# Kernel tuning notes

Hardware: AMD Instinct MI355X
Metric: run time of the kernel (lower is better)

The kernel has to match this reference:

```python
import jax, jax.numpy as jnp
import numpy as np

B, S, D = 2, 2048, 4096
H, KV, HD = 32, 8, 128
THETA = 10000.0


def rotate_half(x):
    x1, x2 = x[..., : HD // 2], x[..., HD // 2 :]
    return jnp.concatenate((-x2, x1), axis=-1)


def setup_inputs() -> dict:
    key = jax.random.key(0)
    ks = jax.random.split(key, 8)
    s = 1.0 / np.sqrt(D)
    return {
        "hidden_states": jax.random.normal(ks[0], (B, S, D), jnp.float32),
        "modality_indicators": jax.random.randint(ks[1], (B, S), 0, 2, jnp.int64 if jax.config.jax_enable_x64 else jnp.int32),
        "position_ids": jnp.arange(S, dtype=jnp.int32),
        "Wq": jax.random.normal(ks[2], (D, H * HD), jnp.float32) * s,
        "Wk0": jax.random.normal(ks[3], (D, KV * HD), jnp.float32) * s,
        "Wk1": jax.random.normal(ks[4], (D, KV * HD), jnp.float32) * s,
        "Wv0": jax.random.normal(ks[5], (D, KV * HD), jnp.float32) * s,
        "Wv1": jax.random.normal(ks[6], (D, KV * HD), jnp.float32) * s,
        "Wo": jax.random.normal(ks[7], (H * HD, D), jnp.float32) * s,
    }


def reference(hidden_states, modality_indicators, position_ids, Wq, Wk0, Wk1, Wv0, Wv1, Wo):
    x = hidden_states
    # Multiway (modality-routed) k/v projections: per-token select between two linears.
    sel = (modality_indicators == 1)[..., None]  # [B,S,1]
    q = x @ Wq                                   # [B,S,H*HD]
    k = jnp.where(sel, x @ Wk1, x @ Wk0)         # [B,S,KV*HD]
    v = jnp.where(sel, x @ Wv1, x @ Wv0)

    q = q.reshape(B, S, H, HD).transpose(0, 2, 1, 3)    # [B,H,S,HD]
    k = k.reshape(B, S, KV, HD).transpose(0, 2, 1, 3)   # [B,KV,S,HD]
    v = v.reshape(B, S, KV, HD).transpose(0, 2, 1, 3)

    # RoPE cache and application (emb = cat(freqs, freqs))
    inv_freq = 1.0 / (THETA ** (jnp.arange(0, HD, 2, dtype=jnp.float32) / HD))
    freqs = position_ids.astype(jnp.float32)[:, None] * inv_freq[None, :]   # [S,HD/2]
    emb = jnp.concatenate((freqs, freqs), axis=-1)                          # [S,HD]
    cos = jnp.cos(emb)[None, None, :, :]                                    # [1,1,S,HD]
    sin = jnp.sin(emb)[None, None, :, :]
    q = q * cos + rotate_half(q) * sin
    k = k * cos + rotate_half(k) * sin

    # GQA: repeat kv heads
    n_rep = H // KV
    k = jnp.repeat(k, n_rep, axis=1)  # [B,H,S,HD]
    v = jnp.repeat(v, n_rep, axis=1)

    scores = jnp.einsum("bhqd,bhkd->bhqk", q, k) / np.sqrt(HD)
    causal = jnp.tril(jnp.ones((S, S), dtype=bool))
    scores = jnp.where(causal[None, None], scores, jnp.finfo(scores.dtype).min)
    attn = jax.nn.softmax(scores, axis=-1)
    ctx = jnp.einsum("bhqk,bhkd->bhqd", attn, v)            # [B,H,S,HD]
    ctx = ctx.transpose(0, 2, 1, 3).reshape(B, S, H * HD)
    return ctx @ Wo
```

## Files before the change

kernel.cpp:

```cpp
#include <hip/hip_runtime.h>

typedef unsigned short u16;
typedef unsigned int   u32;
using bf16x8 = __attribute__((ext_vector_type(8))) __bf16;
using f32x4  = __attribute__((ext_vector_type(4))) float;
using f32x16 = __attribute__((ext_vector_type(16))) float;
using u32x4  = __attribute__((ext_vector_type(4))) unsigned int;


__device__ __forceinline__ u16 f2bf(float f) {
  u32 u = __builtin_bit_cast(u32, f);
  return (u16)((u + 0x7fffu + ((u >> 16) & 1u)) >> 16);
}
__device__ __forceinline__ float bf2f(u16 h) {
  return __builtin_bit_cast(float, (u32)h << 16);
}
__device__ __forceinline__ f32x4 mfma16(bf16x8 a, bf16x8 b, f32x4 c) {
  return __builtin_amdgcn_mfma_f32_16x16x32_bf16(a, b, c, 0, 0, 0);
}
__device__ __forceinline__ f32x16 mfma32(bf16x8 a, bf16x8 b, f32x16 c) {
  return __builtin_amdgcn_mfma_f32_32x32x16_bf16(a, b, c, 0, 0, 0);
}
__device__ __forceinline__ f32x16 zero16() {
  f32x16 z;
#pragma unroll
  for (int i = 0; i < 16; ++i) z[i] = 0.f;
  return z;
}
__device__ __forceinline__ void g2l16(const void* gp, void* lp) {
  __builtin_amdgcn_global_load_lds(
      (__attribute__((address_space(1))) void*)(void*)gp,
      (__attribute__((address_space(3))) void*)lp, 16, 0, 0);
}

__global__ void k_cvt(const float* __restrict__ in, u16* __restrict__ out, int n4) {
  int i = blockIdx.x * 256 + threadIdx.x;
  if (i >= n4) return;
  float4 v = ((const float4*)in)[i];
  ushort4 o;
  o.x = f2bf(v.x); o.y = f2bf(v.y); o.z = f2bf(v.z); o.w = f2bf(v.w);
  ((ushort4*)out)[i] = o;
}

__global__ void k_tcvt(const float* __restrict__ in, u16* __restrict__ out, int K, int N) {
  __shared__ u16 t[32][33];
  int n0 = blockIdx.x * 32, k0 = blockIdx.y * 32;
  int r = threadIdx.x >> 3, c4 = (threadIdx.x & 7) * 4;
  float4 v = *(const float4*)(in + (size_t)(k0 + r) * N + n0 + c4);
  t[c4 + 0][r] = f2bf(v.x);
  t[c4 + 1][r] = f2bf(v.y);
  t[c4 + 2][r] = f2bf(v.z);
  t[c4 + 3][r] = f2bf(v.w);
  __syncthreads();
  ushort4 o;
  o.x = t[r][c4 + 0]; o.y = t[r][c4 + 1]; o.z = t[r][c4 + 2]; o.w = t[r][c4 + 3];
  *(ushort4*)(out + (size_t)(n0 + r) * K + k0 + c4) = o;
}

__global__ void k_scan(const int* __restrict__ mod, int* __restrict__ perm, int* __restrict__ meta) {
  __shared__ int ps[1024];
  const int b = blockIdx.x, t = threadIdx.x;
  perm[b * 2304 + t] = -1;
  perm[b * 2304 + 1024 + t] = -1;
  if (t < 256) perm[b * 2304 + 2048 + t] = -1;
  const int i0 = 2 * t, i1 = 2 * t + 1;
  const int f0 = (mod[b * 2048 + i0] != 1) ? 1 : 0;
  const int f1 = (mod[b * 2048 + i1] != 1) ? 1 : 0;
  const int sum = f0 + f1;
  ps[t] = sum;
  __syncthreads();
  for (int off = 1; off < 1024; off <<= 1) {
    int v = (t >= off) ? ps[t - off] : 0;
    __syncthreads();
    ps[t] += v;
    __syncthreads();
  }
  const int total0 = ps[1023];
  const int excl = ps[t] - sum;
  const int nt0 = (total0 + 255) >> 8;
  const int off1 = nt0 * 256;
  const int s0 = f0 ? excl : off1 + (i0 - excl);
  const int s1 = f1 ? (excl + f0) : off1 + (i1 - (excl + f0));
  perm[b * 2304 + s0] = i0;
  perm[b * 2304 + s1] = i1;
  if (t == 0) { meta[b * 2] = total0; meta[b * 2 + 1] = nt0; }
}

#define TILE_BODY(T, VMLIT, DOSTAGE)                                         \
  {                                                                          \
    asm volatile("s_waitcnt vmcnt(" VMLIT ")" ::: "memory");                 \
    __builtin_amdgcn_s_barrier();                                            \
    __builtin_amdgcn_sched_barrier(0);                                       \
    const u16* base_ = lds + ((T) & 3) * 16384;                              \
    bf16x8 bfr[4], afr[4];                                                   \
    _Pragma("unroll")                                                        \
    for (int nf = 0; nf < 4; ++nf)                                           \
      bfr[nf] = *(const bf16x8*)(base_ + boff + nf * 512);                   \
    _Pragma("unroll")                                                        \
    for (int mf = 0; mf < 4; ++mf)                                           \
      afr[mf] = *(const bf16x8*)(base_ + aoff + mf * 512);                   \
    if (DOSTAGE) stage((T) + 3);                                             \
    __builtin_amdgcn_s_setprio(1);                                           \
    _Pragma("unroll")                                                        \
    for (int mf = 0; mf < 4; ++mf)                                           \
      _Pragma("unroll")                                                      \
      for (int nf = 0; nf < 4; ++nf)                                         \
        acc[mf][nf] = mfma16(afr[mf], bfr[nf], acc[mf][nf]);                 \
    __builtin_amdgcn_s_setprio(0);                                           \
    _Pragma("unroll")                                                        \
    for (int mf = 0; mf < 4; ++mf)                                           \
      afr[mf] = *(const bf16x8*)(base_ + aoff + (mf + 4) * 512);             \
    __builtin_amdgcn_s_setprio(1);                                           \
    _Pragma("unroll")                                                        \
    for (int mf = 0; mf < 4; ++mf)                                           \
      _Pragma("unroll")                                                      \
      for (int nf = 0; nf < 4; ++nf)                                         \
        acc[mf + 4][nf] = mfma16(afr[mf], bfr[nf], acc[mf + 4][nf]);         \
    __builtin_amdgcn_s_setprio(0);                                           \
  }

template <int MODE>
__global__ __launch_bounds__(512, 2) void k_gemm8(const u16* __restrict__ A, const u16* __restrict__ Bt,
                                                  void* __restrict__ Cp, int NH) {
  __shared__ u16 lds[4 * 16384];
  const int tid = threadIdx.x, wid = tid >> 6, l = tid & 63, g = l >> 4, li = l & 15;
  const int wr = wid >> 2, wc = wid & 3;
  const int bid = blockIdx.x;
  const int swz = (bid & 7) * 32 + (bid >> 3);
  const int m0 = (swz >> 4) * 256, n0 = (swz & 15) * 256;

  const int bo = wid * 2048 + l * 16;
  const int srow = bo >> 6;
  const int sgg = (l & 3) ^ ((l >> 3) & 3);
  const u16* ApA = A + (size_t)(m0 + srow) * 4096 + sgg * 8;
  const u16* ApB = Bt + (size_t)(n0 + srow) * 4096 + sgg * 8;

  auto stage = [&](int t) {
    const u16* a = ApA + t * 32;
    const u16* b = ApB + t * 32;
    u16* da = (u16*)lds + (t & 3) * 16384 + wid * 1024;
    u16* db = da + 8192;
    g2l16(a, da);
    g2l16(a + (size_t)16 * 4096, da + 512);
    g2l16(b, db);
    g2l16(b + (size_t)16 * 4096, db + 512);
  };

  const int lsl8 = (g ^ ((li >> 1) & 3)) * 8;
  const int aoff = (wr * 128 + li) * 32 + lsl8;
  const int boff = 8192 + (wc * 64 + li) * 32 + lsl8;

  const f32x4 vzero = {0.f, 0.f, 0.f, 0.f};
  f32x4 acc[8][4];
#pragma unroll
  for (int m = 0; m < 8; ++m)
#pragma unroll
    for (int n = 0; n < 4; ++n) acc[m][n] = vzero;

  stage(0); stage(1); stage(2);
  for (int t = 0; t < 125; ++t) TILE_BODY(t, "8", true);
  TILE_BODY(125, "8", false);
  TILE_BODY(126, "4", false);
  TILE_BODY(127, "0", false);

  (void)NH;
#pragma unroll
  for (int mf = 0; mf < 8; ++mf)
#pragma unroll
    for (int nf = 0; nf < 4; ++nf)
#pragma unroll
      for (int j = 0; j < 4; ++j) {
        int row = m0 + wr * 128 + mf * 16 + g * 4 + j;
        int col = n0 + wc * 64 + nf * 16 + li;
        float v = acc[mf][nf][j];
        if constexpr (MODE == 2) {
          ((float*)Cp)[(size_t)row * 4096 + col] = v;
        } else if constexpr (MODE == 1) {
          int b = row >> 11, s = row & 2047, h = col >> 7, d = col & 127;
          ((u16*)Cp)[(((size_t)(b * NH + h)) * 2048 + s) * 128 + d] = f2bf(v);
        }
      }
}

__global__ __launch_bounds__(512, 2) void k_gemmkv(const u16* __restrict__ Xb,
                                                   const u16* __restrict__ B0, const u16* __restrict__ B1,
                                                   const int* __restrict__ perm, const int* __restrict__ meta,
                                                   u16* __restrict__ Ksel, u16* __restrict__ Vsel) {
  __shared__ u16 lds[4 * 16384];
  const int tid = threadIdx.x, wid = tid >> 6, l = tid & 63, g = l >> 4, li = l & 15;
  const int wr = wid >> 2, wc = wid & 3;
  const int bb = blockIdx.y / 9, tm = blockIdx.y % 9;
  const int n0 = blockIdx.x * 256;
  const int nt0 = meta[bb * 2 + 1];
  const u16* Bt = (tm >= nt0) ? B1 : B0;

  const int bo = wid * 2048 + l * 16;
  const int srow = bo >> 6;
  const int sgg = (l & 3) ^ ((l >> 3) & 3);
  int t0 = perm[bb * 2304 + tm * 256 + srow];
  int t1 = perm[bb * 2304 + tm * 256 + srow + 16];
  if (t0 < 0) t0 = 0;
  if (t1 < 0) t1 = 0;
  const u16* ApA0 = Xb + ((size_t)bb * 2048 + t0) * 4096 + sgg * 8;
  const u16* ApA1 = Xb + ((size_t)bb * 2048 + t1) * 4096 + sgg * 8;
  const u16* ApB = Bt + (size_t)(n0 + srow) * 4096 + sgg * 8;

  auto stage = [&](int t) {
    u16* da = (u16*)lds + (t & 3) * 16384 + wid * 1024;
    u16* db = da + 8192;
    g2l16(ApA0 + t * 32, da);
    g2l16(ApA1 + t * 32, da + 512);
    g2l16(ApB + t * 32, db);
    g2l16(ApB + (size_t)16 * 4096 + t * 32, db + 512);
  };

  const int lsl8 = (g ^ ((li >> 1) & 3)) * 8;
  const int aoff = (wr * 128 + li) * 32 + lsl8;
  const int boff = 8192 + (wc * 64 + li) * 32 + lsl8;

  const f32x4 vzero = {0.f, 0.f, 0.f, 0.f};
  f32x4 acc[8][4];
#pragma unroll
  for (int m = 0; m < 8; ++m)
#pragma unroll
    for (int n = 0; n < 4; ++n) acc[m][n] = vzero;

  stage(0); stage(1); stage(2);
  for (int t = 0; t < 125; ++t) TILE_BODY(t, "8", true);
  TILE_BODY(125, "8", false);
  TILE_BODY(126, "4", false);
  TILE_BODY(127, "0", false);

#pragma unroll
  for (int mf = 0; mf < 8; ++mf)
#pragma unroll
    for (int nf = 0; nf < 4; ++nf)
#pragma unroll
      for (int j = 0; j < 4; ++j) {
        int slot = tm * 256 + wr * 128 + mf * 16 + g * 4 + j;
        int tok = perm[bb * 2304 + slot];
        if (tok >= 0) {
          int col = n0 + wc * 64 + nf * 16 + li;
          int kv = col >> 10, hh = (col >> 7) & 7, d = col & 127;
          u16* dst = (kv ? Vsel : Ksel) + (((size_t)(bb * 8 + hh)) * 2048 + tok) * 128 + d;
          *dst = f2bf(acc[mf][nf][j]);
        }
      }
}

__global__ void k_ropeq(u16* __restrict__ Q, const int* __restrict__ pos) {
  int row = blockIdx.x * 4 + (threadIdx.x >> 6);
  int l = threadIdx.x & 63;
  int s = row & 2047;
  u16* p = Q + (size_t)row * 128;
  float x1 = bf2f(p[l]), x2 = bf2f(p[l + 64]);
  float ang = (float)pos[s] * expf((float)l * -0.14391156831212787f);
  float cs = cosf(ang), sn = sinf(ang);
  const float sc = 0.08838834764831845f;
  p[l] = f2bf((x1 * cs - x2 * sn) * sc);
  p[l + 64] = f2bf((x2 * cs + x1 * sn) * sc);
}

__global__ void k_kvprep(const u16* __restrict__ Ks, const u16* __restrict__ Vs,
                         const int* __restrict__ pos,
                         u16* __restrict__ Kr, u16* __restrict__ Vt) {
  __shared__ u16 Vl[64][136];
  int blk = blockIdx.x;
  int st = blk & 31, kvh = (blk >> 5) & 7, b = blk >> 8;
  int s0 = st * 64;
  int tid = threadIdx.x, wid = tid >> 6, l = tid & 63;
  float invf = expf((float)l * -0.14391156831212787f);
  size_t slab = (size_t)(b * 8 + kvh) * 2048;
  for (int rr = 0; rr < 16; ++rr) {
    int r = wid * 16 + rr;
    int s = s0 + r;
    const u16* ks = Ks + (slab + s) * 128;
    const u16* vs = Vs + (slab + s) * 128;
    float ang = (float)pos[s] * invf;
    float cs = cosf(ang), sn = sinf(ang);
    float x1 = bf2f(ks[l]), x2 = bf2f(ks[l + 64]);
    u16* kd = Kr + (slab + s) * 128;
    kd[l] = f2bf(x1 * cs - x2 * sn);
    kd[l + 64] = f2bf(x2 * cs + x1 * sn);
    Vl[r][l] = vs[l];
    Vl[r][l + 64] = vs[l + 64];
  }
  __syncthreads();
  int d = tid >> 1, si0 = (tid & 1) * 32;
  u16* vd = Vt + ((size_t)(b * 8 + kvh) * 128 + d) * 2048 + s0 + si0;
#pragma unroll
  for (int k4 = 0; k4 < 8; ++k4) {
    ushort4 o;
    o.x = Vl[si0 + k4 * 4 + 0][d];
    o.y = Vl[si0 + k4 * 4 + 1][d];
    o.z = Vl[si0 + k4 * 4 + 2][d];
    o.w = Vl[si0 + k4 * 4 + 3][d];
    *(ushort4*)(vd + k4 * 4) = o;
  }
}

__global__ __launch_bounds__(256, 2) void k_attn(const u16* __restrict__ Q, const u16* __restrict__ Kr,
                                                 const u16* __restrict__ Vt, u16* __restrict__ ctx) {
  __shared__ u16 Kl[2 * 64 * 128];
  __shared__ u16 Vl[2 * 128 * 64];
  const int bh = blockIdx.x;
  const int p = blockIdx.y;
  const int b = bh >> 5, h = bh & 31, kvh = h >> 2;
  const int tid = threadIdx.x, w = tid >> 6, l = tid & 63;
  const int lo5 = l & 31, hi = l >> 5;
  const bool hib = hi != 0;
  const size_t kvslab = (size_t)(b * 8 + kvh) * 2048;
  const u16* Kg = Kr + kvslab * 128;
  const u16* Vg = Vt + kvslab * 128;
  const float L2E = 1.4426950408889634f;

  auto stage = [&](int kt, int bi) {
#pragma unroll
    for (int i = 0; i < 4; ++i) {
      int c = w * 4 + i;
      int slot = c * 1024 + l * 16;
      {
        int row = slot >> 8;
        int inner = (slot & 255) ^ ((row & 15) << 4);
        g2l16((const char*)Kg + kt * 16384 + row * 256 + inner,
              (char*)Kl + bi * 16384 + c * 1024);
      }
      {
        int row = slot >> 7;
        int inner = (slot & 127) ^ ((row & 7) << 4);
        g2l16((const char*)Vg + (size_t)row * 4096 + kt * 128 + inner,
              (char*)Vl + bi * 16384 + c * 1024);
      }
    }
  };

  for (int hf = 0; hf < 2; ++hf) {
    const int qi = hf ? (15 - p) : p;
    const int q0 = qi * 128;
    const int qlane = q0 + w * 32 + lo5;
    const u16* qrow = Q + ((size_t)bh * 2048 + qlane) * 128;
    bf16x8 qf[8];
#pragma unroll
    for (int kk = 0; kk < 8; ++kk) qf[kk] = *(const bf16x8*)(qrow + kk * 16 + hi * 8);

    f32x16 ot[4];
#pragma unroll
    for (int i = 0; i < 4; ++i) ot[i] = zero16();
    float m = -1e30f, ls = 0.f;

    const int nkt = 2 * qi + 2;
    stage(0, 0);
    __syncthreads();
    int cur = 0;
    for (int kt = 0; kt < nkt; ++kt) {
      if (kt + 1 < nkt) stage(kt + 1, cur ^ 1);
      const char* kbase = (const char*)Kl + cur * 16384;
      const char* vbase = (const char*)Vl + cur * 16384;
      const int ktb = kt * 64;
      if (ktb <= q0 + w * 32 + 31) {
        f32x16 st[2];
        st[0] = zero16(); st[1] = zero16();
#pragma unroll
        for (int kk = 0; kk < 8; ++kk) {
          bf16x8 kfr[2];
#pragma unroll
          for (int mf = 0; mf < 2; ++mf) {
            int row = mf * 32 + lo5;
            kfr[mf] = *(const bf16x8*)(kbase + row * 256 + ((kk * 32 + hi * 16) ^ ((row & 15) << 4)));
          }
          __builtin_amdgcn_s_setprio(1);
          st[0] = mfma32(kfr[0], qf[kk], st[0]);
          st[1] = mfma32(kfr[1], qf[kk], st[1]);
          __builtin_amdgcn_s_setprio(0);
        }
        if (ktb + 63 > q0 + w * 32) {
#pragma unroll
          for (int mf = 0; mf < 2; ++mf)
#pragma unroll
            for (int r = 0; r < 16; ++r) {
              int kg = ktb + mf * 32 + (r & 3) + 8 * (r >> 2) + 4 * hi;
              if (kg > qlane) st[mf][r] = -3.0e38f;
            }
        }
        float t[16];
#pragma unroll
        for (int r = 0; r < 16; ++r) t[r] = fmaxf(st[0][r], st[1][r]);
#pragma unroll
        for (int s = 8; s >= 1; s >>= 1)
#pragma unroll
          for (int r = 0; r < s; ++r) t[r] = fmaxf(t[r], t[r + s]);
        float pmax = fmaxf(t[0], __shfl_xor(t[0], 32));
        if (!__all(pmax <= m + 8.f)) {
          float nm = fmaxf(m, pmax);
          float resc = exp2f((m - nm) * L2E);
          m = nm;
          ls *= resc;
#pragma unroll
          for (int i = 0; i < 4; ++i)
#pragma unroll
            for (int r = 0; r < 16; ++r) ot[i][r] *= resc;
        }
#pragma unroll
        for (int mf = 0; mf < 2; ++mf)
#pragma unroll
          for (int r = 0; r < 16; ++r) st[mf][r] = exp2f((st[mf][r] - m) * L2E);
        float u[16];
#pragma unroll
        for (int r = 0; r < 16; ++r) u[r] = st[0][r] + st[1][r];
#pragma unroll
        for (int s = 8; s >= 1; s >>= 1)
#pragma unroll
          for (int r = 0; r < s; ++r) u[r] += u[r + s];
        ls += u[0] + __shfl_xor(u[0], 32);
        u32 pkv[16];
#pragma unroll
        for (int mf = 0; mf < 2; ++mf)
#pragma unroll
          for (int tt = 0; tt < 8; ++tt) {
            u32 r;
            asm("v_cvt_pk_bf16_f32 %0, %1, %2" : "=v"(r) : "v"(st[mf][2 * tt]), "v"(st[mf][2 * tt + 1]));
            pkv[mf * 8 + tt] = r;
          }
        bf16x8 pfrag[4];
#pragma unroll
        for (int kk = 0; kk < 4; ++kk) {
          int c = (kk >> 1) * 8 + (kk & 1) * 4;
          u32 m0 = hib ? pkv[c + 2] : pkv[c + 0];
          u32 m1 = hib ? pkv[c + 3] : pkv[c + 1];
          u32 s0 = hib ? pkv[c + 0] : pkv[c + 2];
          u32 s1 = hib ? pkv[c + 1] : pkv[c + 3];
          u32 r0 = (u32)__shfl_xor((int)s0, 32);
          u32 r1 = (u32)__shfl_xor((int)s1, 32);
          u32x4 wv = {hib ? r0 : m0, hib ? r1 : m1, hib ? m0 : r0, hib ? m1 : r1};
          pfrag[kk] = __builtin_bit_cast(bf16x8, wv);
        }
#pragma unroll
        for (int mfV = 0; mfV < 4; ++mfV) {
          int row = mfV * 32 + lo5;
          const char* vb = vbase + row * 128;
          int sw = (row & 7) << 4;
          bf16x8 vf[4];
#pragma unroll
          for (int kk = 0; kk < 4; ++kk)
            vf[kk] = *(const bf16x8*)(vb + ((kk * 32 + hi * 16) ^ sw));
          __builtin_amdgcn_s_setprio(1);
#pragma unroll
          for (int kk = 0; kk < 4; ++kk) ot[mfV] = mfma32(vf[kk], pfrag[kk], ot[mfV]);
          __builtin_amdgcn_s_setprio(0);
        }
      }
      __syncthreads();
      cur ^= 1;
    }
    float inv = 1.0f / ls;
    u16* crow = ctx + ((size_t)(b * 2048) + qlane) * 4096 + h * 128;
#pragma unroll
    for (int mfV = 0; mfV < 4; ++mfV)
#pragma unroll
      for (int rq = 0; rq < 4; ++rq) {
        ushort4 o4;
        o4.x = f2bf(ot[mfV][rq * 4 + 0] * inv);
        o4.y = f2bf(ot[mfV][rq * 4 + 1] * inv);
        o4.z = f2bf(ot[mfV][rq * 4 + 2] * inv);
        o4.w = f2bf(ot[mfV][rq * 4 + 3] * inv);
        *(ushort4*)(crow + mfV * 32 + rq * 8 + hi * 4) = o4;
      }
  }
}

extern "C" void kernel_launch(void* const* d_in, const int* in_sizes, int n_in,
                              void* d_out, int out_size, void* d_ws, size_t ws_size,
                              hipStream_t stream) {
  (void)in_sizes; (void)n_in; (void)out_size; (void)ws_size;
  const float* X   = (const float*)d_in[0];
  const int*   mod = (const int*)d_in[1];
  const int*   pos = (const int*)d_in[2];
  const float* Wq  = (const float*)d_in[3];
  const float* Wk0 = (const float*)d_in[4];
  const float* Wk1 = (const float*)d_in[5];
  const float* Wv0 = (const float*)d_in[6];
  const float* Wv1 = (const float*)d_in[7];
  const float* Wo  = (const float*)d_in[8];
  float* out = (float*)d_out;

  u16* p = (u16*)d_ws;
  auto take = [&](size_t n) { u16* r = p; p += n; return r; };
  u16* Xb    = take(16777216);
  u16* WqT   = take(16777216);
  u16* WoT   = take(16777216);
  u16* Wkv0T = take(8388608);
  u16* Wkv1T = take(8388608);
  u16* Qr    = take(16777216);
  u16* Ksel  = take(4194304);
  u16* Vsel  = take(4194304);
  int* perm  = (int*)take(9216);
  int* meta  = (int*)take(64);
  u16* Kr  = WqT;
  u16* Vtr = WqT + 4194304;
  u16* ctx = Xb;

  k_cvt<<<dim3(16384), 256, 0, stream>>>(X, Xb, 4194304);
  k_scan<<<dim3(2), 1024, 0, stream>>>(mod, perm, meta);
  k_tcvt<<<dim3(128, 128), 256, 0, stream>>>(Wq, WqT, 4096, 4096);
  k_tcvt<<<dim3(32, 128), 256, 0, stream>>>(Wk0, Wkv0T,                4096, 1024);
  k_tcvt<<<dim3(32, 128), 256, 0, stream>>>(Wv0, Wkv0T + 1024 * 4096,  4096, 1024);
  k_tcvt<<<dim3(32, 128), 256, 0, stream>>>(Wk1, Wkv1T,                4096, 1024);
  k_tcvt<<<dim3(32, 128), 256, 0, stream>>>(Wv1, Wkv1T + 1024 * 4096,  4096, 1024);
  k_tcvt<<<dim3(128, 128), 256, 0, stream>>>(Wo, WoT, 4096, 4096);

  k_gemm8<1><<<dim3(256), 512, 0, stream>>>(Xb, WqT, (void*)Qr, 32);
  k_gemmkv<<<dim3(8, 18), 512, 0, stream>>>(Xb, Wkv0T, Wkv1T, perm, meta, Ksel, Vsel);

  k_ropeq<<<dim3(32768), 256, 0, stream>>>(Qr, pos);
  k_kvprep<<<dim3(512), 256, 0, stream>>>(Ksel, Vsel, pos, Kr, Vtr);

  k_attn<<<dim3(64, 8), 256, 0, stream>>>(Qr, Kr, Vtr, ctx);

  k_gemm8<2><<<dim3(256), 512, 0, stream>>>(ctx, WoT, (void*)out, 0);
}
```

Before: 585.1 us.

## Merge Q and routed KV GEMMs into one launch; deepen attention K/V prefetch

```diff
diff --git a/kernel.cpp b/kernel.cpp
--- a/kernel.cpp
+++ b/kernel.cpp
@@ -119,9 +119,15 @@
     __builtin_amdgcn_s_setprio(0);                                           \
   }
 
-template <int MODE>
+#define GEMM_MAIN_LOOP()                                                     \
+  stage(0); stage(1); stage(2);                                              \
+  for (int t = 0; t < 125; ++t) TILE_BODY(t, "8", true);                     \
+  TILE_BODY(125, "8", false);                                                \
+  TILE_BODY(126, "4", false);                                                \
+  TILE_BODY(127, "0", false);
+
 __global__ __launch_bounds__(512, 2) void k_gemm8(const u16* __restrict__ A, const u16* __restrict__ Bt,
-                                                  void* __restrict__ Cp, int NH) {
+                                                  float* __restrict__ Cp) {
   __shared__ u16 lds[4 * 16384];
   const int tid = threadIdx.x, wid = tid >> 6, l = tid & 63, g = l >> 4, li = l & 15;
   const int wr = wid >> 2, wc = wid & 3;
@@ -132,18 +138,18 @@
   const int bo = wid * 2048 + l * 16;
   const int srow = bo >> 6;
   const int sgg = (l & 3) ^ ((l >> 3) & 3);
-  const u16* ApA = A + (size_t)(m0 + srow) * 4096 + sgg * 8;
-  const u16* ApB = Bt + (size_t)(n0 + srow) * 4096 + sgg * 8;
+  const u16* pA0 = A + (size_t)(m0 + srow) * 4096 + sgg * 8;
+  const u16* pA1 = pA0 + (size_t)16 * 4096;
+  const u16* pB0 = Bt + (size_t)(n0 + srow) * 4096 + sgg * 8;
+  const u16* pB1 = pB0 + (size_t)16 * 4096;
 
   auto stage = [&](int t) {
-    const u16* a = ApA + t * 32;
-    const u16* b = ApB + t * 32;
     u16* da = (u16*)lds + (t & 3) * 16384 + wid * 1024;
     u16* db = da + 8192;
-    g2l16(a, da);
-    g2l16(a + (size_t)16 * 4096, da + 512);
-    g2l16(b, db);
-    g2l16(b + (size_t)16 * 4096, db + 512);
+    g2l16(pA0 + t * 32, da);
+    g2l16(pA1 + t * 32, da + 512);
+    g2l16(pB0 + t * 32, db);
+    g2l16(pB1 + t * 32, db + 512);
   };
 
   const int lsl8 = (g ^ ((li >> 1) & 3)) * 8;
@@ -157,13 +163,8 @@
 #pragma unroll
     for (int n = 0; n < 4; ++n) acc[m][n] = vzero;
 
-  stage(0); stage(1); stage(2);
-  for (int t = 0; t < 125; ++t) TILE_BODY(t, "8", true);
-  TILE_BODY(125, "8", false);
-  TILE_BODY(126, "4", false);
-  TILE_BODY(127, "0", false);
-
-  (void)NH;
+  GEMM_MAIN_LOOP();
+
 #pragma unroll
   for (int mf = 0; mf < 8; ++mf)
 #pragma unroll
@@ -172,46 +173,57 @@
       for (int j = 0; j < 4; ++j) {
         int row = m0 + wr * 128 + mf * 16 + g * 4 + j;
         int col = n0 + wc * 64 + nf * 16 + li;
-        float v = acc[mf][nf][j];
-        if constexpr (MODE == 2) {
-          ((float*)Cp)[(size_t)row * 4096 + col] = v;
-        } else if constexpr (MODE == 1) {
-          int b = row >> 11, s = row & 2047, h = col >> 7, d = col & 127;
-          ((u16*)Cp)[(((size_t)(b * NH + h)) * 2048 + s) * 128 + d] = f2bf(v);
-        }
+        Cp[(size_t)row * 4096 + col] = acc[mf][nf][j];
       }
 }
 
-__global__ __launch_bounds__(512, 2) void k_gemmkv(const u16* __restrict__ Xb,
-                                                   const u16* __restrict__ B0, const u16* __restrict__ B1,
-                                                   const int* __restrict__ perm, const int* __restrict__ meta,
-                                                   u16* __restrict__ Ksel, u16* __restrict__ Vsel) {
+__global__ __launch_bounds__(512, 2) void k_gemmQKV(const u16* __restrict__ Xb, const u16* __restrict__ WqT,
+                                                    const u16* __restrict__ B0, const u16* __restrict__ B1,
+                                                    const int* __restrict__ perm, const int* __restrict__ meta,
+                                                    u16* __restrict__ Qr, u16* __restrict__ Ksel,
+                                                    u16* __restrict__ Vsel) {
   __shared__ u16 lds[4 * 16384];
   const int tid = threadIdx.x, wid = tid >> 6, l = tid & 63, g = l >> 4, li = l & 15;
   const int wr = wid >> 2, wc = wid & 3;
-  const int bb = blockIdx.y / 9, tm = blockIdx.y % 9;
-  const int n0 = blockIdx.x * 256;
-  const int nt0 = meta[bb * 2 + 1];
-  const u16* Bt = (tm >= nt0) ? B1 : B0;
+  const int bid = blockIdx.x;
+  const bool isQ = bid < 256;
 
   const int bo = wid * 2048 + l * 16;
   const int srow = bo >> 6;
   const int sgg = (l & 3) ^ ((l >> 3) & 3);
-  int t0 = perm[bb * 2304 + tm * 256 + srow];
-  int t1 = perm[bb * 2304 + tm * 256 + srow + 16];
-  if (t0 < 0) t0 = 0;
-  if (t1 < 0) t1 = 0;
-  const u16* ApA0 = Xb + ((size_t)bb * 2048 + t0) * 4096 + sgg * 8;
-  const u16* ApA1 = Xb + ((size_t)bb * 2048 + t1) * 4096 + sgg * 8;
-  const u16* ApB = Bt + (size_t)(n0 + srow) * 4096 + sgg * 8;
+
+  int m0 = 0, n0 = 0, bb = 0, tm = 0;
+  const u16 *pA0, *pA1, *pB0;
+  if (isQ) {
+    const int swz = (bid & 7) * 32 + (bid >> 3);
+    m0 = (swz >> 4) * 256; n0 = (swz & 15) * 256;
+    pA0 = Xb + (size_t)(m0 + srow) * 4096 + sgg * 8;
+    pA1 = pA0 + (size_t)16 * 4096;
+    pB0 = WqT + (size_t)(n0 + srow) * 4096 + sgg * 8;
+  } else {
+    const int kb = bid - 256;
+    const int seg = kb >> 3;
+    n0 = (kb & 7) * 256;
+    bb = seg / 9; tm = seg % 9;
+    const int nt0 = meta[bb * 2 + 1];
+    const u16* Bt = (tm >= nt0) ? B1 : B0;
+    int t0 = perm[bb * 2304 + tm * 256 + srow];
+    int t1 = perm[bb * 2304 + tm * 256 + srow + 16];
+    if (t0 < 0) t0 = 0;
+    if (t1 < 0) t1 = 0;
+    pA0 = Xb + ((size_t)bb * 2048 + t0) * 4096 + sgg * 8;
+    pA1 = Xb + ((size_t)bb * 2048 + t1) * 4096 + sgg * 8;
+    pB0 = Bt + (size_t)(n0 + srow) * 4096 + sgg * 8;
+  }
+  const u16* pB1 = pB0 + (size_t)16 * 4096;
 
   auto stage = [&](int t) {
     u16* da = (u16*)lds + (t & 3) * 16384 + wid * 1024;
     u16* db = da + 8192;
-    g2l16(ApA0 + t * 32, da);
-    g2l16(ApA1 + t * 32, da + 512);
-    g2l16(ApB + t * 32, db);
-    g2l16(ApB + (size_t)16 * 4096 + t * 32, db + 512);
+    g2l16(pA0 + t * 32, da);
+    g2l16(pA1 + t * 32, da + 512);
+    g2l16(pB0 + t * 32, db);
+    g2l16(pB1 + t * 32, db + 512);
   };
 
   const int lsl8 = (g ^ ((li >> 1) & 3)) * 8;
@@ -225,27 +237,37 @@
 #pragma unroll
     for (int n = 0; n < 4; ++n) acc[m][n] = vzero;
 
-  stage(0); stage(1); stage(2);
-  for (int t = 0; t < 125; ++t) TILE_BODY(t, "8", true);
-  TILE_BODY(125, "8", false);
-  TILE_BODY(126, "4", false);
-  TILE_BODY(127, "0", false);
-
-#pragma unroll
-  for (int mf = 0; mf < 8; ++mf)
-#pragma unroll
-    for (int nf = 0; nf < 4; ++nf)
-#pragma unroll
-      for (int j = 0; j < 4; ++j) {
-        int slot = tm * 256 + wr * 128 + mf * 16 + g * 4 + j;
-        int tok = perm[bb * 2304 + slot];
-        if (tok >= 0) {
+  GEMM_MAIN_LOOP();
+
+  if (isQ) {
+#pragma unroll
+    for (int mf = 0; mf < 8; ++mf)
+#pragma unroll
+      for (int nf = 0; nf < 4; ++nf)
+#pragma unroll
+        for (int j = 0; j < 4; ++j) {
+          int row = m0 + wr * 128 + mf * 16 + g * 4 + j;
           int col = n0 + wc * 64 + nf * 16 + li;
-          int kv = col >> 10, hh = (col >> 7) & 7, d = col & 127;
-          u16* dst = (kv ? Vsel : Ksel) + (((size_t)(bb * 8 + hh)) * 2048 + tok) * 128 + d;
-          *dst = f2bf(acc[mf][nf][j]);
-        }
-      }
+          int b = row >> 11, s = row & 2047, h = col >> 7, d = col & 127;
+          Qr[(((size_t)(b * 32 + h)) * 2048 + s) * 128 + d] = f2bf(acc[mf][nf][j]);
+        }
+  } else {
+#pragma unroll
+    for (int mf = 0; mf < 8; ++mf)
+#pragma unroll
+      for (int nf = 0; nf < 4; ++nf)
+#pragma unroll
+        for (int j = 0; j < 4; ++j) {
+          int slot = tm * 256 + wr * 128 + mf * 16 + g * 4 + j;
+          int tok = perm[bb * 2304 + slot];
+          if (tok >= 0) {
+            int col = n0 + wc * 64 + nf * 16 + li;
+            int kv = col >> 10, hh = (col >> 7) & 7, d = col & 127;
+            u16* dst = (kv ? Vsel : Ksel) + (((size_t)(bb * 8 + hh)) * 2048 + tok) * 128 + d;
+            *dst = f2bf(acc[mf][nf][j]);
+          }
+        }
+  }
 }
 
 __global__ void k_ropeq(u16* __restrict__ Q, const int* __restrict__ pos) {
@@ -350,12 +372,17 @@
 
     const int nkt = 2 * qi + 2;
     stage(0, 0);
-    __syncthreads();
-    int cur = 0;
+    stage(1, 1);
     for (int kt = 0; kt < nkt; ++kt) {
-      if (kt + 1 < nkt) stage(kt + 1, cur ^ 1);
-      const char* kbase = (const char*)Kl + cur * 16384;
-      const char* vbase = (const char*)Vl + cur * 16384;
+      if (kt + 1 < nkt) {
+        asm volatile("s_waitcnt vmcnt(8)" ::: "memory");
+      } else {
+        asm volatile("s_waitcnt vmcnt(0)" ::: "memory");
+      }
+      __builtin_amdgcn_s_barrier();
+      __builtin_amdgcn_sched_barrier(0);
+      const char* kbase = (const char*)Kl + (kt & 1) * 16384;
+      const char* vbase = (const char*)Vl + (kt & 1) * 16384;
       const int ktb = kt * 64;
       if (ktb <= q0 + w * 32 + 31) {
         f32x16 st[2];
@@ -449,8 +476,8 @@
           __builtin_amdgcn_s_setprio(0);
         }
       }
-      __syncthreads();
-      cur ^= 1;
+      __builtin_amdgcn_s_barrier();
+      if (kt + 2 < nkt) stage(kt + 2, kt & 1);
     }
     float inv = 1.0f / ls;
     u16* crow = ctx + ((size_t)(b * 2048) + qlane) * 4096 + h * 128;
@@ -508,13 +535,12 @@
   k_tcvt<<<dim3(32, 128), 256, 0, stream>>>(Wv1, Wkv1T + 1024 * 4096,  4096, 1024);
   k_tcvt<<<dim3(128, 128), 256, 0, stream>>>(Wo, WoT, 4096, 4096);
 
-  k_gemm8<1><<<dim3(256), 512, 0, stream>>>(Xb, WqT, (void*)Qr, 32);
-  k_gemmkv<<<dim3(8, 18), 512, 0, stream>>>(Xb, Wkv0T, Wkv1T, perm, meta, Ksel, Vsel);
+  k_gemmQKV<<<dim3(400), 512, 0, stream>>>(Xb, WqT, Wkv0T, Wkv1T, perm, meta, Qr, Ksel, Vsel);
 
   k_ropeq<<<dim3(32768), 256, 0, stream>>>(Qr, pos);
   k_kvprep<<<dim3(512), 256, 0, stream>>>(Ksel, Vsel, pos, Kr, Vtr);
 
   k_attn<<<dim3(64, 8), 256, 0, stream>>>(Qr, Kr, Vtr, ctx);
 
-  k_gemm8<2><<<dim3(256), 512, 0, stream>>>(ctx, WoT, (void*)out, 0);
-}
+  k_gemm8<<<dim3(256), 512, 0, stream>>>(ctx, WoT, out);
+}
```

New measurement: 570.8 us. -2.4%, faster.
